# Kernel optimization log

Hardware: AMD Instinct MI355X
Metric: run time of the kernel (lower is better)

## Reference

```python
import jax, jax.numpy as jnp
import numpy as np
import math

D_QKV = 64


def setup_inputs() -> dict:
    key = jax.random.key(0)
    ks = jax.random.split(key, 6)
    b, l, d_model, n_head, d_qkv = 2, 2048, 1024, 16, D_QKV
    return {
        "x": jax.random.normal(ks[0], (b, l, d_model), dtype=jnp.float32),
        "w_q": jax.random.normal(ks[1], (n_head, d_model, d_qkv), dtype=jnp.float32) * (2.0 / (d_model + d_qkv)) ** 0.5,
        "w_k": jax.random.normal(ks[2], (n_head, d_model, d_qkv), dtype=jnp.float32) * (2.0 / (d_model + d_qkv)) ** 0.5,
        "w_v": jax.random.normal(ks[3], (n_head, d_model, d_qkv), dtype=jnp.float32) * (2.0 / (d_model + d_qkv)) ** 0.5,
        "w_o": jax.random.normal(ks[4], (n_head, d_qkv, d_model), dtype=jnp.float32) * (2.0 / (d_model + d_qkv)) ** 0.5,
        "mask": jnp.zeros((b, 1, 1, l), dtype=bool),  # True = masked (padding)
    }


def reference(x, w_q, w_k, w_v, w_o, mask):
    # x: [b, l, m]; w_{q,k,v}: [n, m, d]; w_o: [n, d, m]; mask broadcastable to [b, n, l, l]
    q = jnp.einsum("blm,nmd->bnld", x, w_q)
    k = jnp.einsum("blm,nmd->bnld", x, w_k)
    v = jnp.einsum("blm,nmd->bnld", x, w_v)
    scores = jnp.einsum("bnld,bnkd->bnlk", q, k) / math.sqrt(D_QKV)
    scores = jnp.where(mask, jnp.float32(-1e9), scores)
    attn = jax.nn.softmax(scores, axis=-1)  # dropout is identity (p=0 / eval)
    ctx = jnp.einsum("bnlk,bnkd->bnld", attn, v)
    # per-head output projection then sum over heads: V.matmul(w_o).sum(dim=1)
    return jnp.einsum("bnld,ndm->blm", ctx, w_o)
```

## Files before the change

### kernel.cpp

```cpp
#include <hip/hip_runtime.h>
#include <stdint.h>

using bf16x8  = __attribute__((ext_vector_type(8))) short;
using f32x4   = __attribute__((ext_vector_type(4))) float;
using f32x16  = __attribute__((ext_vector_type(16))) float;
using ushort8 = __attribute__((ext_vector_type(8))) unsigned short;
using ushort4v= __attribute__((ext_vector_type(4))) unsigned short;
using uint2v  = __attribute__((ext_vector_type(2))) unsigned int;

typedef __attribute__((address_space(1))) const unsigned int* gas_ptr;
typedef __attribute__((address_space(3))) unsigned int*       las_ptr;

__device__ __forceinline__ void gload_lds16(const unsigned short* g, unsigned short* l) {
    __builtin_amdgcn_global_load_lds((gas_ptr)(const void*)g, (las_ptr)(void*)l, 16, 0, 0);
}

__device__ __forceinline__ unsigned short f2bf(float f) {
    union { float f; uint32_t u; } x; x.f = f;
    uint32_t u = x.u;
    uint32_t r = u + 0x7fffu + ((u >> 16) & 1u);
    return (unsigned short)(r >> 16);
}

__device__ __forceinline__ f32x4 mfma16(bf16x8 a, bf16x8 b, f32x4 c) {
    return __builtin_amdgcn_mfma_f32_16x16x32_bf16(a, b, c, 0, 0, 0);
}
__device__ __forceinline__ f32x16 mfma32(bf16x8 a, bf16x8 b, f32x16 c) {
    return __builtin_amdgcn_mfma_f32_32x32x16_bf16(a, b, c, 0, 0, 0);
}

__device__ __forceinline__ unsigned int cvtpk_bf16(float lo, float hi) {
    unsigned int r;
    asm("v_cvt_pk_bf16_f32 %0, %1, %2" : "=v"(r) : "v"(lo), "v"(hi));
    return r;
}
__device__ __forceinline__ void plswap(unsigned int& a, unsigned int& b) {
    asm("v_permlane32_swap_b32 %0, %1" : "+v"(a), "+v"(b));
}


__global__ void cast_x_kernel(const float* __restrict__ x, unsigned short* __restrict__ xb) {
    int i = blockIdx.x * 256 + threadIdx.x;
    using f32x4v = __attribute__((ext_vector_type(4))) float;
    f32x4v v = ((const f32x4v*)x)[i];
    ushort4v o;
    o[0] = f2bf(v[0]); o[1] = f2bf(v[1]); o[2] = f2bf(v[2]); o[3] = f2bf(v[3]);
    ((ushort4v*)xb)[i] = o;
}

__global__ void pack_wqkv_kernel(const float* __restrict__ wq, const float* __restrict__ wk,
                                 const float* __restrict__ wv, unsigned short* __restrict__ wpT) {
    int idx = blockIdx.x * 256 + threadIdx.x;
    int kk = idx & 1023;
    int j  = idx >> 10;
    int s  = j >> 10, rem = j & 1023;
    int hh = rem >> 6, dd = rem & 63;
    const float* src = (s == 0) ? wq : (s == 1) ? wk : wv;
    wpT[idx] = f2bf(src[((size_t)hh * 1024 + kk) * 64 + dd]);
}

__global__ void pack_wo_kernel(const float* __restrict__ wo, unsigned short* __restrict__ woT) {
    int idx = blockIdx.x * 256 + threadIdx.x;
    int kk = idx & 1023;
    int m  = idx >> 10;
    woT[idx] = f2bf(wo[(size_t)kk * 1024 + m]);
}


template<int MODE, int BN>
__global__ __launch_bounds__(256) void gemm_bt(
    const unsigned short* __restrict__ A,
    const unsigned short* __restrict__ BT,
    float* __restrict__ Cf,
    unsigned short* __restrict__ Q,
    unsigned short* __restrict__ Kq,
    unsigned short* __restrict__ V,
    int M, int N, int K)
{
    constexpr int NF = BN / 32;
    __shared__ unsigned short As[128 * 64];
    __shared__ unsigned short Bs[BN * 64];
    const int tid  = threadIdx.x;
    const int lane = tid & 63;
    const int wave = tid >> 6;
    const int wm = wave >> 1, wn = wave & 1;
    const int l15 = lane & 15, l4 = lane >> 4;
    const int row0 = blockIdx.y * 128;
    const int col0 = blockIdx.x * BN;

    f32x4 acc[4][NF];
#pragma unroll
    for (int i = 0; i < 4; ++i)
#pragma unroll
        for (int j = 0; j < NF; ++j) acc[i][j] = (f32x4){0.f, 0.f, 0.f, 0.f};

    for (int k0 = 0; k0 < K; k0 += 64) {
        __syncthreads();
#pragma unroll
        for (int it = 0; it < 4; ++it) {
            int cb = (it * 4 + wave) * 64;
            int c  = cb + lane;
            int r  = c >> 3, c8 = c & 7;
            int sc8 = c8 ^ (r & 7);
            gload_lds16(&A[(size_t)(row0 + r) * K + k0 + sc8 * 8], &As[cb * 8]);
        }
#pragma unroll
        for (int it = 0; it < NF; ++it) {
            int cb = (it * 4 + wave) * 64;
            int c  = cb + lane;
            int r  = c >> 3, c8 = c & 7;
            int sc8 = c8 ^ (r & 7);
            gload_lds16(&BT[(size_t)(col0 + r) * K + k0 + sc8 * 8], &Bs[cb * 8]);
        }
        __syncthreads();
#pragma unroll
        for (int kk = 0; kk < 2; ++kk) {
            bf16x8 af[4], bfr[NF];
#pragma unroll
            for (int m = 0; m < 4; ++m) {
                int r   = wm * 64 + m * 16 + l15;
                int blk = (kk * 4 + l4) ^ (r & 7);
                af[m] = *(const bf16x8*)&As[r * 64 + blk * 8];
            }
#pragma unroll
            for (int n = 0; n < NF; ++n) {
                int r   = wn * (BN / 2) + n * 16 + l15;
                int blk = (kk * 4 + l4) ^ (r & 7);
                bfr[n] = *(const bf16x8*)&Bs[r * 64 + blk * 8];
            }
#pragma unroll
            for (int m = 0; m < 4; ++m)
#pragma unroll
                for (int n = 0; n < NF; ++n)
                    acc[m][n] = mfma16(af[m], bfr[n], acc[m][n]);
        }
    }

#pragma unroll
    for (int m = 0; m < 4; ++m) {
#pragma unroll
        for (int n = 0; n < NF; ++n) {
#pragma unroll
            for (int r = 0; r < 4; ++r) {
                int gr = row0 + wm * 64 + m * 16 + l4 * 4 + r;
                int gc = col0 + wn * (BN / 2) + n * 16 + l15;
                float v = acc[m][n][r];
                if (MODE == 0) {
                    int s = gc >> 10, rem = gc & 1023;
                    int hh = rem >> 6, dd = rem & 63;
                    int bb = gr >> 11, ll = gr & 2047;
                    unsigned short* dst = (s == 0) ? Q : (s == 1) ? Kq : V;
                    dst[(((size_t)bb * 16 + hh) * 2048 + ll) * 64 + dd] = f2bf(v);
                } else {
                    Cf[(size_t)gr * N + gc] = v;
                }
            }
        }
    }
}


__global__ __launch_bounds__(256) void attn_kernel(
    const unsigned short* __restrict__ qb,
    const unsigned short* __restrict__ kb,
    const unsigned short* __restrict__ vb,
    const unsigned char* __restrict__ mask,
    unsigned short* __restrict__ ctxb)
{
    const int lg  = blockIdx.x;
    const int swz = ((lg & 7) << 6) | (lg >> 3);
    const int qt = swz & 15, h = (swz >> 4) & 15, b = swz >> 8;

    const int tid  = threadIdx.x;
    const int lane = tid & 63, wave = tid >> 6;
    const int l31  = lane & 31, hi = lane >> 5;

    __shared__ unsigned short smem[16384];
    __shared__ int flags[32];

    const size_t hoff = ((size_t)(b * 16 + h)) * 2048 * 64;
    const unsigned short* qh = qb + hoff;
    const unsigned short* kh = kb + hoff;
    const unsigned short* vh = vb + hoff;
    const unsigned char*  mb = mask + (size_t)b * 2048;

    if (tid < 32) flags[tid] = 0;
    __syncthreads();
    {
        uint2v mv = *(const uint2v*)&mb[tid * 8];
        if (mv[0] | mv[1]) flags[tid >> 3] = 1;
    }

    const int qrow = qt * 128 + wave * 32 + l31;
    bf16x8 qf[4];
#pragma unroll
    for (int ki = 0; ki < 4; ++ki)
        qf[ki] = *(const bf16x8*)&qh[(size_t)qrow * 64 + ki * 16 + hi * 8];

    f32x16 accA = {0,0,0,0,0,0,0,0,0,0,0,0,0,0,0,0};
    f32x16 accB = {0,0,0,0,0,0,0,0,0,0,0,0,0,0,0,0};
    float m_r = -1e30f, l_r = 0.f;
    const float SC  = 0.18033688011112042f;
    const float THR = 44.3614195558365f;

    const int krow = tid >> 3, kc16 = tid & 7;
    const int vd = tid & 63, vcb = (tid >> 6) * 2;

    ushort8 kreg[2];
    unsigned short vreg[16];
#pragma unroll
    for (int it = 0; it < 2; ++it)
        kreg[it] = *(const ushort8*)&kh[(size_t)(krow + it * 32) * 64 + kc16 * 8];
#pragma unroll
    for (int j = 0; j < 16; ++j)
        vreg[j] = vh[(size_t)(vcb * 8 + j) * 64 + vd];

    for (int t = 0; t < 32; ++t) {
        const int kv0 = t * 64;
        unsigned short* Kb = smem + (t & 1) * 4096;
        unsigned short* Vb = smem + 8192 + (t & 1) * 4096;

#pragma unroll
        for (int it = 0; it < 2; ++it) {
            int r = krow + it * 32;
            *(ushort8*)&Kb[r * 64 + ((kc16 ^ (r & 7)) * 8)] = kreg[it];
        }
        {
            union { unsigned short u[16]; ushort8 v[2]; } p;
#pragma unroll
            for (int j = 0; j < 16; ++j) p.u[j] = vreg[j];
#pragma unroll
            for (int c = 0; c < 2; ++c) {
                int cc = vcb + c;
                *(ushort8*)&Vb[vd * 64 + ((cc ^ (vd & 7)) * 8)] = p.v[c];
            }
        }
        __syncthreads();

        if (t < 31) {
            const int kvn = kv0 + 64;
#pragma unroll
            for (int it = 0; it < 2; ++it)
                kreg[it] = *(const ushort8*)&kh[(size_t)(kvn + krow + it * 32) * 64 + kc16 * 8];
#pragma unroll
            for (int j = 0; j < 16; ++j)
                vreg[j] = vh[(size_t)(kvn + vcb * 8 + j) * 64 + vd];
        }

        f32x16 s0 = {0,0,0,0,0,0,0,0,0,0,0,0,0,0,0,0};
        f32x16 s1 = {0,0,0,0,0,0,0,0,0,0,0,0,0,0,0,0};
        __builtin_amdgcn_s_setprio(1);
#pragma unroll
        for (int ki = 0; ki < 4; ++ki) {
            int c0 = ((ki * 2 + hi) ^ (l31 & 7)) * 8;
            bf16x8 a0 = *(const bf16x8*)&Kb[l31 * 64 + c0];
            bf16x8 a1 = *(const bf16x8*)&Kb[(32 + l31) * 64 + c0];
            s0 = mfma32(a0, qf[ki], s0);
            s1 = mfma32(a1, qf[ki], s1);
        }
        __builtin_amdgcn_s_setprio(0);

        if (flags[t]) {
#pragma unroll
            for (int r = 0; r < 16; ++r) {
                int keyl = (r & 3) + 8 * (r >> 2) + 4 * hi;
                if (mb[kv0 + keyl])      s0[r] = -1e30f;
                if (mb[kv0 + 32 + keyl]) s1[r] = -1e30f;
            }
        }

        float mx;
        {
            float a0 = fmaxf(fmaxf(s0[0], s0[1]),  fmaxf(s0[2],  s0[3]));
            float a1 = fmaxf(fmaxf(s0[4], s0[5]),  fmaxf(s0[6],  s0[7]));
            float a2 = fmaxf(fmaxf(s0[8], s0[9]),  fmaxf(s0[10], s0[11]));
            float a3 = fmaxf(fmaxf(s0[12], s0[13]), fmaxf(s0[14], s0[15]));
            float b0 = fmaxf(fmaxf(s1[0], s1[1]),  fmaxf(s1[2],  s1[3]));
            float b1 = fmaxf(fmaxf(s1[4], s1[5]),  fmaxf(s1[6],  s1[7]));
            float b2 = fmaxf(fmaxf(s1[8], s1[9]),  fmaxf(s1[10], s1[11]));
            float b3 = fmaxf(fmaxf(s1[12], s1[13]), fmaxf(s1[14], s1[15]));
            mx = fmaxf(fmaxf(fmaxf(a0, a1), fmaxf(a2, a3)),
                       fmaxf(fmaxf(b0, b1), fmaxf(b2, b3)));
        }
        mx = fmaxf(mx, __shfl_xor(mx, 32));
        if (__any(mx > m_r + THR)) {
            float mn  = fmaxf(m_r, mx);
            float scl = __builtin_amdgcn_exp2f((m_r - mn) * SC);
            m_r = mn;
            l_r *= scl;
#pragma unroll
            for (int i = 0; i < 16; ++i) { accA[i] *= scl; accB[i] *= scl; }
        }
        const float nmc = -m_r * SC;
#pragma unroll
        for (int i = 0; i < 16; ++i) {
            s0[i] = __builtin_amdgcn_exp2f(__builtin_fmaf(s0[i], SC, nmc));
            s1[i] = __builtin_amdgcn_exp2f(__builtin_fmaf(s1[i], SC, nmc));
        }
        float rs;
        {
            float a0 = (s0[0] + s0[1]) + (s0[2] + s0[3]);
            float a1 = (s0[4] + s0[5]) + (s0[6] + s0[7]);
            float a2 = (s0[8] + s0[9]) + (s0[10] + s0[11]);
            float a3 = (s0[12] + s0[13]) + (s0[14] + s0[15]);
            float b0 = (s1[0] + s1[1]) + (s1[2] + s1[3]);
            float b1 = (s1[4] + s1[5]) + (s1[6] + s1[7]);
            float b2 = (s1[8] + s1[9]) + (s1[10] + s1[11]);
            float b3 = (s1[12] + s1[13]) + (s1[14] + s1[15]);
            rs = ((a0 + a1) + (a2 + a3)) + ((b0 + b1) + (b2 + b3));
        }
        rs += __shfl_xor(rs, 32);
        l_r += rs;

        bf16x8 pf[4];
        {
            union { unsigned int u[4]; bf16x8 v; } f;
            unsigned int w0 = cvtpk_bf16(s0[0],  s0[1]),  w1 = cvtpk_bf16(s0[2],  s0[3]);
            unsigned int w2 = cvtpk_bf16(s0[4],  s0[5]),  w3 = cvtpk_bf16(s0[6],  s0[7]);
            unsigned int w4 = cvtpk_bf16(s0[8],  s0[9]),  w5 = cvtpk_bf16(s0[10], s0[11]);
            unsigned int w6 = cvtpk_bf16(s0[12], s0[13]), w7 = cvtpk_bf16(s0[14], s0[15]);
            plswap(w0, w2); plswap(w1, w3); plswap(w4, w6); plswap(w5, w7);
            f.u[0] = w0; f.u[1] = w1; f.u[2] = w2; f.u[3] = w3; pf[0] = f.v;
            f.u[0] = w4; f.u[1] = w5; f.u[2] = w6; f.u[3] = w7; pf[1] = f.v;
            unsigned int x0 = cvtpk_bf16(s1[0],  s1[1]),  x1 = cvtpk_bf16(s1[2],  s1[3]);
            unsigned int x2 = cvtpk_bf16(s1[4],  s1[5]),  x3 = cvtpk_bf16(s1[6],  s1[7]);
            unsigned int x4 = cvtpk_bf16(s1[8],  s1[9]),  x5 = cvtpk_bf16(s1[10], s1[11]);
            unsigned int x6 = cvtpk_bf16(s1[12], s1[13]), x7 = cvtpk_bf16(s1[14], s1[15]);
            plswap(x0, x2); plswap(x1, x3); plswap(x4, x6); plswap(x5, x7);
            f.u[0] = x0; f.u[1] = x1; f.u[2] = x2; f.u[3] = x3; pf[2] = f.v;
            f.u[0] = x4; f.u[1] = x5; f.u[2] = x6; f.u[3] = x7; pf[3] = f.v;
        }

        __builtin_amdgcn_s_setprio(1);
#pragma unroll
        for (int ks = 0; ks < 4; ++ks) {
            int c0 = ((ks * 2 + hi) ^ (l31 & 7)) * 8;
            bf16x8 vA = *(const bf16x8*)&Vb[l31 * 64 + c0];
            bf16x8 vB = *(const bf16x8*)&Vb[(32 + l31) * 64 + c0];
            accA = mfma32(vA, pf[ks], accA);
            accB = mfma32(vB, pf[ks], accB);
        }
        __builtin_amdgcn_s_setprio(0);
    }

    __syncthreads();
    const float inv = 1.0f / l_r;
    const int qloc = wave * 32 + l31;
#pragma unroll
    for (int r = 0; r < 16; ++r) {
        int dA = (r & 3) + 8 * (r >> 2) + 4 * hi;
        smem[qloc * 64 + (dA ^ ((qloc & 7) * 8))]        = f2bf(accA[r] * inv);
        smem[qloc * 64 + ((32 + dA) ^ ((qloc & 7) * 8))] = f2bf(accB[r] * inv);
    }
    __syncthreads();
#pragma unroll
    for (int it = 0; it < 4; ++it) {
        int idx = tid + it * 256;
        int q = idx >> 3, c = idx & 7;
        ushort8 vv = *(const ushort8*)&smem[q * 64 + ((c * 8) ^ ((q & 7) * 8))];
        *(ushort8*)&ctxb[((size_t)(b * 2048 + qt * 128 + q)) * 1024 + h * 64 + c * 8] = vv;
    }
}


extern "C" void kernel_launch(void* const* d_in, const int* in_sizes, int n_in,
                              void* d_out, int out_size, void* d_ws, size_t ws_size,
                              hipStream_t stream)
{
    const float* x  = (const float*)d_in[0];
    const float* wq = (const float*)d_in[1];
    const float* wk = (const float*)d_in[2];
    const float* wv = (const float*)d_in[3];
    const float* wo = (const float*)d_in[4];
    const unsigned char* mask = (const unsigned char*)d_in[5];
    float* out = (float*)d_out;

    char* ws = (char*)d_ws;
    unsigned short* xb   = (unsigned short*)(ws);
    unsigned short* wpT  = (unsigned short*)(ws + 8388608);
    unsigned short* woT  = (unsigned short*)(ws + 14680064);
    unsigned short* qb   = (unsigned short*)(ws + 16777216);
    unsigned short* kb   = (unsigned short*)(ws + 25165824);
    unsigned short* vb   = (unsigned short*)(ws + 33554432);
    unsigned short* ctxb = (unsigned short*)(ws + 41943040);

    cast_x_kernel   <<<4096, 256, 0, stream>>>(x, xb);
    pack_wqkv_kernel<<<12288, 256, 0, stream>>>(wq, wk, wv, wpT);
    pack_wo_kernel  <<<4096, 256, 0, stream>>>(wo, woT);

    gemm_bt<0,128><<<dim3(24, 32), 256, 0, stream>>>(xb, wpT, nullptr, qb, kb, vb, 4096, 3072, 1024);
    attn_kernel<<<512, 256, 0, stream>>>(qb, kb, vb, mask, ctxb);
    gemm_bt<1,64><<<dim3(16, 32), 256, 0, stream>>>(ctxb, woT, out, nullptr, nullptr, nullptr, 4096, 1024, 1024);
}
```

Measured before the change: 144.3 us.

## Split attention KV range in two with combine pass; tile weight transposes through LDS

The attention kernel can now split each query tile's KV loop into two halves across separate blocks, doubling the grid from 512 to 1024. Each half writes unnormalized bf16 partial outputs plus running max and sum, and a new combine kernel merges them into ctx. The weight pack kernels are rewritten as 64x64 LDS-tiled transposes so both the global reads and the writes are coalesced. The split adds partial-output traffic, an extra launch and an extra bf16 rounding of partials, and it only runs when the workspace is large enough.

```diff
diff --git a/kernel.cpp b/kernel.cpp
--- a/kernel.cpp
+++ b/kernel.cpp
@@ -20,6 +20,10 @@
     uint32_t u = x.u;
     uint32_t r = u + 0x7fffu + ((u >> 16) & 1u);
     return (unsigned short)(r >> 16);
+}
+__device__ __forceinline__ float bf2f(unsigned short u) {
+    union { uint32_t u; float f; } x; x.u = ((uint32_t)u) << 16;
+    return x.f;
 }
 
 __device__ __forceinline__ f32x4 mfma16(bf16x8 a, bf16x8 b, f32x4 c) {
@@ -48,22 +52,46 @@
     ((ushort4v*)xb)[i] = o;
 }
 
-__global__ void pack_wqkv_kernel(const float* __restrict__ wq, const float* __restrict__ wk,
-                                 const float* __restrict__ wv, unsigned short* __restrict__ wpT) {
-    int idx = blockIdx.x * 256 + threadIdx.x;
-    int kk = idx & 1023;
-    int j  = idx >> 10;
-    int s  = j >> 10, rem = j & 1023;
-    int hh = rem >> 6, dd = rem & 63;
-    const float* src = (s == 0) ? wq : (s == 1) ? wk : wv;
-    wpT[idx] = f2bf(src[((size_t)hh * 1024 + kk) * 64 + dd]);
-}
-
-__global__ void pack_wo_kernel(const float* __restrict__ wo, unsigned short* __restrict__ woT) {
-    int idx = blockIdx.x * 256 + threadIdx.x;
-    int kk = idx & 1023;
-    int m  = idx >> 10;
-    woT[idx] = f2bf(wo[(size_t)kk * 1024 + m]);
+__global__ void pack_wqkv_t(const float* __restrict__ wq, const float* __restrict__ wk,
+                            const float* __restrict__ wv, unsigned short* __restrict__ wpT) {
+    __shared__ float tile[64][65];
+    const int mm = blockIdx.y;
+    const int s = mm >> 4, hh = mm & 15;
+    const float* src = ((s == 0) ? wq : (s == 1) ? wk : wv) + (size_t)hh * 1024 * 64;
+    const int k0 = blockIdx.x * 64;
+    const int c = threadIdx.x & 63, rg = threadIdx.x >> 6;
+#pragma unroll
+    for (int i = 0; i < 16; ++i) {
+        int r = rg * 16 + i;
+        tile[r][c] = src[(size_t)(k0 + r) * 64 + c];
+    }
+    __syncthreads();
+    unsigned short* dst = wpT + ((size_t)s * 1024 + hh * 64) * 1024 + k0;
+    const int kc = threadIdx.x & 63, dg = threadIdx.x >> 6;
+#pragma unroll
+    for (int i = 0; i < 16; ++i) {
+        int d = dg * 16 + i;
+        dst[(size_t)d * 1024 + kc] = f2bf(tile[kc][d]);
+    }
+}
+
+__global__ void pack_wo_t(const float* __restrict__ wo, unsigned short* __restrict__ woT) {
+    __shared__ float tile[64][65];
+    const int r0 = blockIdx.y * 64;
+    const int c0 = blockIdx.x * 64;
+    const int c = threadIdx.x & 63, rg = threadIdx.x >> 6;
+#pragma unroll
+    for (int i = 0; i < 16; ++i) {
+        int r = rg * 16 + i;
+        tile[r][c] = wo[(size_t)(r0 + r) * 1024 + c0 + c];
+    }
+    __syncthreads();
+    const int kc = threadIdx.x & 63, mg = threadIdx.x >> 6;
+#pragma unroll
+    for (int i = 0; i < 16; ++i) {
+        int m = mg * 16 + i;
+        woT[(size_t)(c0 + m) * 1024 + r0 + kc] = f2bf(tile[kc][m]);
+    }
 }
 
 
@@ -160,16 +188,30 @@
 }
 
 
+template<int SPLIT>
 __global__ __launch_bounds__(256) void attn_kernel(
     const unsigned short* __restrict__ qb,
     const unsigned short* __restrict__ kb,
     const unsigned short* __restrict__ vb,
     const unsigned char* __restrict__ mask,
-    unsigned short* __restrict__ ctxb)
+    unsigned short* __restrict__ ctxb,
+    unsigned short* __restrict__ part,
+    float* __restrict__ ml)
 {
-    const int lg  = blockIdx.x;
-    const int swz = ((lg & 7) << 6) | (lg >> 3);
-    const int qt = swz & 15, h = (swz >> 4) & 15, b = swz >> 8;
+    const int lg = blockIdx.x;
+    int qt, h, b, t0;
+    int half = 0;
+    if (SPLIT) {
+        int u = ((lg & 7) << 7) | (lg >> 3);
+        int bh = u >> 5, sub = u & 31;
+        qt = sub >> 1; half = sub & 1;
+        b = bh >> 4; h = bh & 15;
+        t0 = half * 16;
+    } else {
+        int swz = ((lg & 7) << 6) | (lg >> 3);
+        qt = swz & 15; h = (swz >> 4) & 15; b = swz >> 8; t0 = 0;
+    }
+    const int NT = SPLIT ? 16 : 32;
 
     const int tid  = threadIdx.x;
     const int lane = tid & 63, wave = tid >> 6;
@@ -208,14 +250,17 @@
 
     ushort8 kreg[2];
     unsigned short vreg[16];
-#pragma unroll
-    for (int it = 0; it < 2; ++it)
-        kreg[it] = *(const ushort8*)&kh[(size_t)(krow + it * 32) * 64 + kc16 * 8];
-#pragma unroll
-    for (int j = 0; j < 16; ++j)
-        vreg[j] = vh[(size_t)(vcb * 8 + j) * 64 + vd];
-
-    for (int t = 0; t < 32; ++t) {
+    {
+        const int kvb = t0 * 64;
+#pragma unroll
+        for (int it = 0; it < 2; ++it)
+            kreg[it] = *(const ushort8*)&kh[(size_t)(kvb + krow + it * 32) * 64 + kc16 * 8];
+#pragma unroll
+        for (int j = 0; j < 16; ++j)
+            vreg[j] = vh[(size_t)(kvb + vcb * 8 + j) * 64 + vd];
+    }
+
+    for (int t = t0; t < t0 + NT; ++t) {
         const int kv0 = t * 64;
         unsigned short* Kb = smem + (t & 1) * 4096;
         unsigned short* Vb = smem + 8192 + (t & 1) * 4096;
@@ -237,7 +282,7 @@
         }
         __syncthreads();
 
-        if (t < 31) {
+        if (t < t0 + NT - 1) {
             const int kvn = kv0 + 64;
 #pragma unroll
             for (int it = 0; it < 2; ++it)
@@ -344,22 +389,59 @@
     }
 
     __syncthreads();
-    const float inv = 1.0f / l_r;
     const int qloc = wave * 32 + l31;
+    const float inv = SPLIT ? 1.0f : (1.0f / l_r);
 #pragma unroll
     for (int r = 0; r < 16; ++r) {
         int dA = (r & 3) + 8 * (r >> 2) + 4 * hi;
         smem[qloc * 64 + (dA ^ ((qloc & 7) * 8))]        = f2bf(accA[r] * inv);
         smem[qloc * 64 + ((32 + dA) ^ ((qloc & 7) * 8))] = f2bf(accB[r] * inv);
     }
+    if (SPLIT && hi == 0) {
+        size_t mrow = ((size_t)half * 32 + b * 16 + h) * 2048 + qt * 128 + qloc;
+        *(float2*)&ml[mrow * 2] = make_float2(m_r, l_r);
+    }
     __syncthreads();
-#pragma unroll
-    for (int it = 0; it < 4; ++it) {
-        int idx = tid + it * 256;
-        int q = idx >> 3, c = idx & 7;
-        ushort8 vv = *(const ushort8*)&smem[q * 64 + ((c * 8) ^ ((q & 7) * 8))];
-        *(ushort8*)&ctxb[((size_t)(b * 2048 + qt * 128 + q)) * 1024 + h * 64 + c * 8] = vv;
-    }
+    if (SPLIT) {
+        const size_t prow0 = ((size_t)half * 32 + (b * 16 + h)) * 2048 + qt * 128;
+#pragma unroll
+        for (int it = 0; it < 4; ++it) {
+            int idx = tid + it * 256;
+            int q = idx >> 3, c = idx & 7;
+            ushort8 vv = *(const ushort8*)&smem[q * 64 + ((c * 8) ^ ((q & 7) * 8))];
+            *(ushort8*)&part[(prow0 + q) * 64 + c * 8] = vv;
+        }
+    } else {
+#pragma unroll
+        for (int it = 0; it < 4; ++it) {
+            int idx = tid + it * 256;
+            int q = idx >> 3, c = idx & 7;
+            ushort8 vv = *(const ushort8*)&smem[q * 64 + ((c * 8) ^ ((q & 7) * 8))];
+            *(ushort8*)&ctxb[((size_t)(b * 2048 + qt * 128 + q)) * 1024 + h * 64 + c * 8] = vv;
+        }
+    }
+}
+
+
+__global__ void combine_kernel(const unsigned short* __restrict__ part,
+                               const float* __restrict__ ml,
+                               unsigned short* __restrict__ ctxb)
+{
+    const float SC = 0.18033688011112042f;
+    int gid = blockIdx.x * 256 + threadIdx.x;
+    int row = gid >> 6, d = gid & 63;
+    float p0 = bf2f(part[(size_t)row * 64 + d]);
+    float p1 = bf2f(part[(size_t)(65536 + row) * 64 + d]);
+    float2 a = *(const float2*)&ml[(size_t)row * 2];
+    float2 c = *(const float2*)&ml[(size_t)(65536 + row) * 2];
+    float m  = fmaxf(a.x, c.x);
+    float w0 = __builtin_amdgcn_exp2f((a.x - m) * SC);
+    float w1 = __builtin_amdgcn_exp2f((c.x - m) * SC);
+    float l  = a.y * w0 + c.y * w1;
+    float o  = (p0 * w0 + p1 * w1) / l;
+    int bh = row >> 11, ql = row & 2047;
+    int bb = bh >> 4, hh = bh & 15;
+    ctxb[((size_t)(bb * 2048 + ql)) * 1024 + hh * 64 + d] = f2bf(o);
 }
 
 
@@ -383,12 +465,22 @@
     unsigned short* kb   = (unsigned short*)(ws + 25165824);
     unsigned short* vb   = (unsigned short*)(ws + 33554432);
     unsigned short* ctxb = (unsigned short*)(ws + 41943040);
-
-    cast_x_kernel   <<<4096, 256, 0, stream>>>(x, xb);
-    pack_wqkv_kernel<<<12288, 256, 0, stream>>>(wq, wk, wv, wpT);
-    pack_wo_kernel  <<<4096, 256, 0, stream>>>(wo, woT);
+    unsigned short* part = (unsigned short*)(ws + 50331648);
+    float*          mlb  = (float*)(ws + 67108864);
+    const bool split = ws_size >= (size_t)68157440;
+
+    cast_x_kernel<<<4096, 256, 0, stream>>>(x, xb);
+    pack_wqkv_t  <<<dim3(16, 48), 256, 0, stream>>>(wq, wk, wv, wpT);
+    pack_wo_t    <<<dim3(16, 16), 256, 0, stream>>>(wo, woT);
 
     gemm_bt<0,128><<<dim3(24, 32), 256, 0, stream>>>(xb, wpT, nullptr, qb, kb, vb, 4096, 3072, 1024);
-    attn_kernel<<<512, 256, 0, stream>>>(qb, kb, vb, mask, ctxb);
+
+    if (split) {
+        attn_kernel<1><<<1024, 256, 0, stream>>>(qb, kb, vb, mask, nullptr, part, mlb);
+        combine_kernel<<<16384, 256, 0, stream>>>(part, mlb, ctxb);
+    } else {
+        attn_kernel<0><<<512, 256, 0, stream>>>(qb, kb, vb, mask, ctxb, nullptr, nullptr);
+    }
+
     gemm_bt<1,64><<<dim3(16, 32), 256, 0, stream>>>(ctxb, woT, out, nullptr, nullptr, nullptr, 4096, 1024, 1024);
 }
```

Result: faster. 139.1 us (-3.6%).
